# Kernel tuning notes

Measured on AMD Instinct MI355X. Metric: run time of the kernel, lower is better.

Reference implementation:

```python
import jax, jax.numpy as jnp
import numpy as np

NEG = -1e9  # finite stand-in for -inf (avoids inf-inf NaNs, safe in fp32)


def setup_inputs() -> dict:
    T, V, Lmax, A = 2048, 8192, 8, 64
    rng = np.random.default_rng(0)
    seq = rng.integers(0, A, size=T).astype(np.int32)
    # first A pieces are the single codepoints -> every sequence is segmentable
    piece_lens = np.concatenate([
        np.ones(A, np.int32),
        rng.integers(1, Lmax + 1, size=V - A).astype(np.int32),
    ])
    pieces = rng.integers(0, A, size=(V, Lmax)).astype(np.int32)
    pieces[:A, 0] = np.arange(A)
    logits = rng.standard_normal(V).astype(np.float32)
    m = logits.max()
    log_probs = (logits - m - np.log(np.exp(logits - m).sum())).astype(np.float32)
    return {
        'seq': jnp.asarray(seq),
        'pieces': jnp.asarray(pieces),
        'piece_lens': jnp.asarray(piece_lens),
        'log_probs': jnp.asarray(log_probs),
    }


def reference(seq, pieces, piece_lens, log_probs):
    T = seq.shape[0]
    V, Lmax = pieces.shape
    dt = log_probs.dtype

    # --- match table: match[t, i] = piece i matches sequence at position t ---
    seq_pad = jnp.concatenate([seq, jnp.full((Lmax,), -1, seq.dtype)])
    windows = seq_pad[jnp.arange(T)[:, None] + jnp.arange(Lmax)[None, :]]  # [T, Lmax]
    lmask = jnp.arange(Lmax)[None, :] < piece_lens[:, None]                # [V, Lmax]
    eq = windows[:, None, :] == pieces[None, :, :]                        # [T, V, Lmax]
    fits = (jnp.arange(T)[:, None] + piece_lens[None, :]) <= T            # [T, V]
    match = jnp.all(eq | ~lmask[None, :, :], axis=-1) & fits              # [T, V]
    mlp = jnp.where(match, log_probs[None, :], NEG).astype(dt)            # [T, V]

    # end_logp[t-1, i] = mlp[t - len_i, i]  (piece i ending exactly at t, t=1..T)
    te = jnp.arange(1, T + 1)[:, None]
    src = te - piece_lens[None, :]
    end_logp = jnp.where(src >= 0,
                         mlp[jnp.clip(src, 0, T - 1), jnp.arange(V)[None, :]],
                         NEG)

    # --- forward pass: alpha[t] = logsumexp_i alpha[t - len_i] + log p_i ---
    idx_a = Lmax - piece_lens  # window slot holding alpha[t - len_i]
    def fstep(win, row):
        a_t = jax.nn.logsumexp(win[idx_a] + row)
        return jnp.concatenate([win[1:], a_t[None]]), a_t
    win0 = jnp.full((Lmax,), NEG, dt).at[-1].set(0.0)
    _, alpha_rest = jax.lax.scan(fstep, win0, end_logp)
    alpha = jnp.concatenate([jnp.zeros((1,), dt), alpha_rest])  # [T+1]

    # --- backward pass: beta[t] = logsumexp_i log p_i + beta[t + len_i] ---
    idx_b = piece_lens - 1  # window slot holding beta[t + len_i]
    def bstep(win, row):
        b_t = jax.nn.logsumexp(row + win[idx_b])
        return jnp.concatenate([b_t[None], win[:-1]]), b_t
    winT = jnp.full((Lmax,), NEG, dt).at[0].set(0.0)
    _, beta_rev = jax.lax.scan(bstep, winT, mlp[::-1])
    beta = jnp.concatenate([beta_rev[::-1], jnp.zeros((1,), dt)])  # [T+1]

    # --- posteriors: P[t, i] = exp(alpha[t] + log p_i + beta[t+len_i] - alpha[T]) ---
    norm = alpha[T]
    beta_next = beta[jnp.clip(jnp.arange(T)[:, None] + piece_lens[None, :], 0, T)]
    P = jnp.exp(alpha[:T][:, None] + mlp + beta_next - norm)
    P = jnp.where(match, P, 0.0)
    return jnp.where(norm > NEG / 2, P, jnp.zeros_like(P))
```

## Files before the change

### kernel.cpp

```cpp
#include <hip/hip_runtime.h>
#include <stdint.h>

#define LMAX 8
#define KCH 32
#define NC  64
#define TT  2048
#define LN2D 0.6931471805599453
#define NEGE (-(1<<28))

struct __align__(16) PK { unsigned long long key; float logp; int len; };

__device__ __forceinline__ int fexp(float m) { return ((__float_as_int(m) >> 23) & 0xFF) - 127; }
__device__ __forceinline__ int fexpbits(float m) { return (__float_as_int(m) >> 23) & 0xFF; }
__device__ __forceinline__ float p2(int e) { return __int_as_float((e + 127) << 23); }
__device__ __forceinline__ float p2c(int e) { return (e < -126) ? 0.f : p2(e); }

__global__ void k_prep(const int* __restrict__ seq, const int* __restrict__ pieces,
                       const int* __restrict__ plens, const float* __restrict__ logp,
                       PK* __restrict__ pk, unsigned long long* __restrict__ w64,
                       float* __restrict__ M, int T, int V) {
  int idx = blockIdx.x * blockDim.x + threadIdx.x;
  if (idx < V) {
    const int* pr = pieces + idx * LMAX;
    int len = plens[idx];
    unsigned long long key = 0ull;
    #pragma unroll
    for (int l = 0; l < LMAX; ++l) {
      unsigned long long b = (unsigned long long)(pr[l] & 0xFF);
      if (l < len) key |= b << (8 * l);
    }
    PK o; o.key = key; o.logp = logp[idx]; o.len = len;
    pk[idx] = o;
  } else if (idx < V + T) {
    int t = idx - V;
    unsigned long long w = 0ull;
    #pragma unroll
    for (int l = 0; l < LMAX; ++l) {
      int pos = t + l;
      unsigned long long b = (pos < T) ? (unsigned long long)(seq[pos] & 0xFF) : 0xFFull;
      w |= b << (8 * l);
    }
    w64[t] = w;
  } else if (idx < V + T + T * LMAX) {
    M[idx - V - T] = 0.f;
  }
}

__global__ void k_match(const PK* __restrict__ pk, const unsigned long long* __restrict__ w64,
                        float* __restrict__ M, int T, int V, int tPer) {
  int v = blockIdx.x * blockDim.x + threadIdx.x;
  PK p = pk[v];
  unsigned long long mask = (p.len >= 8) ? ~0ull : ((1ull << (8 * p.len)) - 1ull);
  unsigned long long key = p.key;
  int t0 = blockIdx.y * tPer;
  float prob = -1.f;
  for (int t = t0; t < t0 + tPer; ++t) {
    unsigned long long w = w64[t];
    if (((w ^ key) & mask) == 0ull) {
      if (prob < 0.f) prob = expf(p.logp);
      atomicAdd(&M[t * LMAX + (p.len - 1)], prob);
    }
  }
}

__global__ __launch_bounds__(512) void k_chunks(const float* __restrict__ M,
        float* __restrict__ Wt, int* __restrict__ EWc) {
  int gtid = blockIdx.x * 512 + threadIdx.x;
  int task = gtid >> 3, b = gtid & 7;
  int dir = task >> 6, c = task & 63;
  int base = c * KCH;
  const float4* Mv = (const float4*)M;
  float v[8];
  #pragma unroll
  for (int i = 0; i < 8; ++i) v[i] = (i == b) ? 1.f : 0.f;
  int ec = 0;
  if (dir == 0) {
    float4 ra = Mv[base * 2], rb = Mv[base * 2 + 1];
    for (int kg = 0; kg < 4; ++kg) {
      #pragma unroll
      for (int kk = 0; kk < 8; ++kk) {
        int k = kg * 8 + kk;
        float4 c0 = ra, c1 = rb;
        int nk = (k + 1 < KCH) ? k + 1 : KCH - 1;
        ra = Mv[(base + nk) * 2]; rb = Mv[(base + nk) * 2 + 1];
        float a_ = v[kk & 7];
        v[(kk + 1) & 7] = fmaf(a_, c0.x, v[(kk + 1) & 7]);
        v[(kk + 2) & 7] = fmaf(a_, c0.y, v[(kk + 2) & 7]);
        v[(kk + 3) & 7] = fmaf(a_, c0.z, v[(kk + 3) & 7]);
        v[(kk + 4) & 7] = fmaf(a_, c0.w, v[(kk + 4) & 7]);
        v[(kk + 5) & 7] = fmaf(a_, c1.x, v[(kk + 5) & 7]);
        v[(kk + 6) & 7] = fmaf(a_, c1.y, v[(kk + 6) & 7]);
        v[(kk + 7) & 7] = fmaf(a_, c1.z, v[(kk + 7) & 7]);
        v[kk & 7]       = a_ * c1.w;
        if (kk == 3 || kk == 7) {
          float mx = 0.f;
          #pragma unroll
          for (int i = 0; i < 8; ++i) mx = fmaxf(mx, v[i]);
          if (fexpbits(mx) != 0) {
            int e = fexp(mx); float sc = p2(-e);
            #pragma unroll
            for (int i = 0; i < 8; ++i) v[i] *= sc;
            ec += e;
          }
        }
      }
    }
  } else {
    float4 ra = Mv[(base + KCH - 1) * 2], rb = Mv[(base + KCH - 1) * 2 + 1];
    for (int kg = 0; kg < 4; ++kg) {
      #pragma unroll
      for (int kk = 0; kk < 8; ++kk) {
        int k = kg * 8 + kk;
        float4 c0 = ra, c1 = rb;
        int nk = (k + 1 < KCH) ? k + 1 : KCH - 1;
        int nt = base + KCH - 1 - nk;
        ra = Mv[nt * 2]; rb = Mv[nt * 2 + 1];
        float nb =      c0.x * v[(8  - kk) & 7];
        nb = fmaf(c0.y, v[(9  - kk) & 7], nb);
        nb = fmaf(c0.z, v[(10 - kk) & 7], nb);
        nb = fmaf(c0.w, v[(11 - kk) & 7], nb);
        nb = fmaf(c1.x, v[(12 - kk) & 7], nb);
        nb = fmaf(c1.y, v[(13 - kk) & 7], nb);
        nb = fmaf(c1.z, v[(14 - kk) & 7], nb);
        nb = fmaf(c1.w, v[(15 - kk) & 7], nb);
        v[(7 - kk) & 7] = nb;
        if (kk == 3 || kk == 7) {
          float mx = 0.f;
          #pragma unroll
          for (int i = 0; i < 8; ++i) mx = fmaxf(mx, v[i]);
          if (fexpbits(mx) != 0) {
            int e = fexp(mx); float sc = p2(-e);
            #pragma unroll
            for (int i = 0; i < 8; ++i) v[i] *= sc;
            ec += e;
          }
        }
      }
    }
  }
  float mx = 0.f;
  #pragma unroll
  for (int i = 0; i < 8; ++i) mx = fmaxf(mx, v[i]);
  int ltask = dir * 64 + (dir ? 63 - c : c);
  float* wp = Wt + ltask * 64;
  if (fexpbits(mx) == 0) {
    #pragma unroll
    for (int i = 0; i < 8; ++i) wp[b * 8 + i] = 0.f;
    EWc[ltask * 8 + b] = NEGE;
  } else {
    int e = fexp(mx); float sc = p2(-e);
    #pragma unroll
    for (int i = 0; i < 8; ++i) wp[b * 8 + i] = v[i] * sc;
    EWc[ltask * 8 + b] = ec + e;
  }
}

__global__ __launch_bounds__(256) void k_combine(const float* __restrict__ Wt,
        const int* __restrict__ EWc, float* __restrict__ Pm,
        float* __restrict__ Cs, int* __restrict__ Eacc) {
  __shared__ float sWt[128][68];
  __shared__ int   sEW[128 * 8];
  __shared__ int   sEP[128 * 8];
  __shared__ float Gm[16 * 69];
  __shared__ float Sg[16 * 9];
  __shared__ int   EGs[16 * 8];
  __shared__ int   EsB[16];
  const int tid = threadIdx.x;

  for (int i = tid; i < 128 * 16; i += 256) {
    int task = i >> 4, q = i & 15;
    float4 v4 = ((const float4*)Wt)[i];
    *(float4*)&sWt[task][q * 4] = v4;
  }
  for (int i = tid; i < 1024; i += 256) sEW[i] = EWc[i];
  __syncthreads();

  if (tid < 128) {
    const int dir = tid >> 6, w = (tid >> 3) & 7, b = tid & 7;
    float v[8];
    #pragma unroll
    for (int i = 0; i < 8; ++i) v[i] = (i == b) ? 1.f : 0.f;
    int ec = 0;
    for (int c = 0; c < 8; ++c) {
      int lc = w * 8 + c, lt = dir * 64 + lc;
      float* pp = Pm + lt * 64 + b * 8;
      #pragma unroll
      for (int i = 0; i < 8; ++i) pp[i] = v[i];
      sEP[lt * 8 + b] = ec;
      const float* wp = &sWt[lt][0];
      int ew[8];
      #pragma unroll
      for (int j = 0; j < 8; ++j) ew[j] = sEW[lt * 8 + j];
      int emax = ew[0];
      #pragma unroll
      for (int j = 1; j < 8; ++j) emax = max(emax, ew[j]);
      float nv[8] = {0, 0, 0, 0, 0, 0, 0, 0};
      #pragma unroll
      for (int j = 0; j < 8; ++j) {
        float tj = v[j] * p2c(ew[j] - emax + 64);
        float4 ca = *(const float4*)(wp + j * 8);
        float4 cb = *(const float4*)(wp + j * 8 + 4);
        nv[0] = fmaf(tj, ca.x, nv[0]); nv[1] = fmaf(tj, ca.y, nv[1]);
        nv[2] = fmaf(tj, ca.z, nv[2]); nv[3] = fmaf(tj, ca.w, nv[3]);
        nv[4] = fmaf(tj, cb.x, nv[4]); nv[5] = fmaf(tj, cb.y, nv[5]);
        nv[6] = fmaf(tj, cb.z, nv[6]); nv[7] = fmaf(tj, cb.w, nv[7]);
      }
      float mx = 0.f;
      #pragma unroll
      for (int i = 0; i < 8; ++i) mx = fmaxf(mx, nv[i]);
      if (fexpbits(mx) == 0) {
        #pragma unroll
        for (int i = 0; i < 8; ++i) v[i] = 0.f;
        ec = NEGE;
      } else {
        int e = fexp(mx); float sc = p2(-e);
        #pragma unroll
        for (int i = 0; i < 8; ++i) v[i] = nv[i] * sc;
        ec = ec + emax + e - 64;
      }
    }
    float* gp = Gm + (dir * 8 + w) * 69 + b * 8;
    #pragma unroll
    for (int i = 0; i < 8; ++i) gp[i] = v[i];
    EGs[(dir * 8 + w) * 8 + b] = ec;
  }
  __syncthreads();

  if (tid < 8 || (tid >= 64 && tid < 72)) {
    const int dir = (tid >= 64) ? 1 : 0, j = tid & 7;
    float s[8];
    #pragma unroll
    for (int i = 0; i < 8; ++i) s[i] = (i == 0) ? 1.f : 0.f;
    int Es = 0;
    for (int w = 0; w < 8; ++w) {
      float sj = s[0];
      #pragma unroll
      for (int i = 1; i < 8; ++i) if (j == i) sj = s[i];
      Sg[(dir * 8 + w) * 9 + j] = sj;
      if (j == 0) EsB[dir * 8 + w] = Es;
      int eg[8];
      #pragma unroll
      for (int i = 0; i < 8; ++i) eg[i] = EGs[(dir * 8 + w) * 8 + i];
      int egmax = eg[0];
      #pragma unroll
      for (int i = 1; i < 8; ++i) egmax = max(egmax, eg[i]);
      int egj = eg[0];
      #pragma unroll
      for (int i = 1; i < 8; ++i) if (j == i) egj = eg[i];
      float tb = sj * p2c(egj - egmax + 64);
      const float* gp = Gm + (dir * 8 + w) * 69 + j * 8;
      float p[8];
      #pragma unroll
      for (int i = 0; i < 8; ++i) p[i] = gp[i] * tb;
      #pragma unroll
      for (int m = 1; m <= 4; m <<= 1)
        #pragma unroll
        for (int i = 0; i < 8; ++i) p[i] += __shfl_xor(p[i], m);
      float mx = 0.f;
      #pragma unroll
      for (int i = 0; i < 8; ++i) mx = fmaxf(mx, p[i]);
      int e = fexp(mx); float sc = p2(-e);
      #pragma unroll
      for (int i = 0; i < 8; ++i) s[i] = p[i] * sc;
      Es += egmax + e - 64;
    }
  }
  __syncthreads();

  if (tid < 128) {
    const int dir = tid >> 6, lc = tid & 63, w = lc >> 3;
    float sg[8];
    #pragma unroll
    for (int b = 0; b < 8; ++b) sg[b] = Sg[(dir * 8 + w) * 9 + b];
    int Es = EsB[dir * 8 + w];
    int ep[8];
    #pragma unroll
    for (int b = 0; b < 8; ++b) ep[b] = sEP[(dir * 64 + lc) * 8 + b];
    int epmax = ep[0];
    #pragma unroll
    for (int b = 1; b < 8; ++b) epmax = max(epmax, ep[b]);
    float cs[8] = {0, 0, 0, 0, 0, 0, 0, 0};
    #pragma unroll
    for (int b = 0; b < 8; ++b) {
      float coef = sg[b] * p2c(ep[b] - epmax + 64);
      const float* pp = Pm + (dir * 64 + lc) * 64 + b * 8;
      float4 ca = *(const float4*)pp;
      float4 cb = *(const float4*)(pp + 4);
      cs[0] = fmaf(coef, ca.x, cs[0]); cs[1] = fmaf(coef, ca.y, cs[1]);
      cs[2] = fmaf(coef, ca.z, cs[2]); cs[3] = fmaf(coef, ca.w, cs[3]);
      cs[4] = fmaf(coef, cb.x, cs[4]); cs[5] = fmaf(coef, cb.y, cs[5]);
      cs[6] = fmaf(coef, cb.z, cs[6]); cs[7] = fmaf(coef, cb.w, cs[7]);
    }
    float mx = 0.f;
    #pragma unroll
    for (int i = 0; i < 8; ++i) mx = fmaxf(mx, cs[i]);
    int phys = dir ? (63 - lc) : lc;
    float* cp = Cs + (dir * 64 + phys) * 8;
    if (fexpbits(mx) == 0) {
      #pragma unroll
      for (int i = 0; i < 8; ++i) cp[i] = 0.f;
      Eacc[dir * 64 + phys] = NEGE;
    } else {
      int e = fexp(mx); float sc = p2(-e);
      #pragma unroll
      for (int i = 0; i < 8; ++i) cp[i] = cs[i] * sc;
      Eacc[dir * 64 + phys] = Es + epmax + e - 64;
    }
  }
}

__global__ __launch_bounds__(64) void k_replay(const float* __restrict__ M,
        const float* __restrict__ Cs, const int* __restrict__ Eacc,
        float* __restrict__ aL, float* __restrict__ bL) {
  const int dir = blockIdx.x;
  const int c = threadIdx.x;
  const int base = c * KCH;
  const float4* Mv = (const float4*)M;
  const float* cp = Cs + (dir * 64 + c) * 8;
  double st[8];
  #pragma unroll
  for (int i = 0; i < 8; ++i) st[i] = (double)cp[i];
  const double eacc = (double)Eacc[dir * 64 + c];
  if (dir == 0) {
    if (c == 0) aL[0] = 0.f;
    float4 ra = Mv[base * 2], rb = Mv[base * 2 + 1];
    for (int kg = 0; kg < 4; ++kg) {
      #pragma unroll
      for (int kk = 0; kk < 8; ++kk) {
        int k = kg * 8 + kk;
        float4 c0 = ra, c1 = rb;
        int nk = (k + 1 < KCH) ? k + 1 : KCH - 1;
        ra = Mv[(base + nk) * 2]; rb = Mv[(base + nk) * 2 + 1];
        double a_ = st[kk & 7];
        st[(kk + 1) & 7] = fma(a_, (double)c0.x, st[(kk + 1) & 7]);
        st[(kk + 2) & 7] = fma(a_, (double)c0.y, st[(kk + 2) & 7]);
        st[(kk + 3) & 7] = fma(a_, (double)c0.z, st[(kk + 3) & 7]);
        st[(kk + 4) & 7] = fma(a_, (double)c0.w, st[(kk + 4) & 7]);
        st[(kk + 5) & 7] = fma(a_, (double)c1.x, st[(kk + 5) & 7]);
        st[(kk + 6) & 7] = fma(a_, (double)c1.y, st[(kk + 6) & 7]);
        st[(kk + 7) & 7] = fma(a_, (double)c1.z, st[(kk + 7) & 7]);
        st[kk & 7]       = a_ * (double)c1.w;
        double val = st[(kk + 1) & 7];
        long long bits = __double_as_longlong(val);
        int e2 = (int)((bits >> 52) & 0x7ff) - 1023;
        double mant = __longlong_as_double((bits & 0xFFFFFFFFFFFFFLL) | 0x3FF0000000000000LL);
        float lg = log2f((float)mant);
        aL[base + k + 1] = (float)(((double)e2 + eacc + (double)lg) * LN2D);
      }
    }
  } else {
    if (c == 0) bL[TT] = 0.f;
    float4 ra = Mv[(base + KCH - 1) * 2], rb = Mv[(base + KCH - 1) * 2 + 1];
    for (int kg = 0; kg < 4; ++kg) {
      #pragma unroll
      for (int kk = 0; kk < 8; ++kk) {
        int k = kg * 8 + kk;
        int t = base + KCH - 1 - k;
        float4 c0 = ra, c1 = rb;
        int nk = (k + 1 < KCH) ? k + 1 : KCH - 1;
        int nt = base + KCH - 1 - nk;
        ra = Mv[nt * 2]; rb = Mv[nt * 2 + 1];
        double nb =            (double)c0.x * st[(8  - kk) & 7];
        nb = fma((double)c0.y, st[(9  - kk) & 7], nb);
        nb = fma((double)c0.z, st[(10 - kk) & 7], nb);
        nb = fma((double)c0.w, st[(11 - kk) & 7], nb);
        nb = fma((double)c1.x, st[(12 - kk) & 7], nb);
        nb = fma((double)c1.y, st[(13 - kk) & 7], nb);
        nb = fma((double)c1.z, st[(14 - kk) & 7], nb);
        nb = fma((double)c1.w, st[(15 - kk) & 7], nb);
        st[(7 - kk) & 7] = nb;
        long long bits = __double_as_longlong(nb);
        int e2 = (int)((bits >> 52) & 0x7ff) - 1023;
        double mant = __longlong_as_double((bits & 0xFFFFFFFFFFFFFLL) | 0x3FF0000000000000LL);
        float lg = log2f((float)mant);
        bL[t] = (float)(((double)e2 + eacc + (double)lg) * LN2D);
      }
    }
  }
}

__global__ void k_out(const PK* __restrict__ pk, const unsigned long long* __restrict__ w64,
                      const float* __restrict__ aL, const float* __restrict__ bL,
                      float* __restrict__ out, int T, int V, int tPer) {
  int v = blockIdx.x * blockDim.x + threadIdx.x;
  PK p = pk[v];
  unsigned long long mask = (p.len >= 8) ? ~0ull : ((1ull << (8 * p.len)) - 1ull);
  unsigned long long key = p.key;
  float norm = aL[T];
  float base = p.logp - norm;
  int t0 = blockIdx.y * tPer;
  for (int t = t0; t < t0 + tPer; ++t) {
    unsigned long long w = w64[t];
    float val = 0.f;
    if (((w ^ key) & mask) == 0ull)
      val = __expf(aL[t] + base + bL[t + p.len]);
    out[(size_t)t * V + v] = val;
  }
}

extern "C" void kernel_launch(void* const* d_in, const int* in_sizes, int n_in,
                              void* d_out, int out_size, void* d_ws, size_t ws_size,
                              hipStream_t stream) {
  const int* seq    = (const int*)d_in[0];
  const int* pieces = (const int*)d_in[1];
  const int* plens  = (const int*)d_in[2];
  const float* logp = (const float*)d_in[3];
  float* out = (float*)d_out;
  const int T = in_sizes[0];
  const int V = in_sizes[2];

  char* p = (char*)d_ws;
  PK* pk = (PK*)p;                                   p += (size_t)V * sizeof(PK);
  unsigned long long* w64 = (unsigned long long*)p;  p += (size_t)T * 8;
  float* M = (float*)p;                              p += (size_t)T * LMAX * 4;
  float* Wt = (float*)p;                             p += (size_t)128 * 64 * 4;
  int* EWc = (int*)p;                                p += (size_t)128 * 8 * 4;
  float* Pm = (float*)p;                             p += (size_t)128 * 64 * 4;
  float* Cs = (float*)p;                             p += (size_t)128 * 8 * 4;
  int* Eacc = (int*)p;                               p += 512;
  float* aL = (float*)p;                             p += 8208;
  float* bL = (float*)p;                             p += 8208;

  int prepN = V + T + T * LMAX;
  k_prep<<<(prepN + 255) / 256, 256, 0, stream>>>(seq, pieces, plens, logp, pk, w64, M, T, V);

  const int tPer2 = 128;
  dim3 g2(V / 256, T / tPer2);
  k_match<<<g2, 256, 0, stream>>>(pk, w64, M, T, V, tPer2);

  k_chunks<<<2, 512, 0, stream>>>(M, Wt, EWc);
  k_combine<<<1, 256, 0, stream>>>(Wt, EWc, Pm, Cs, Eacc);
  k_replay<<<2, 64, 0, stream>>>(M, Cs, Eacc, aL, bL);

  const int tPer5 = 32;
  dim3 g5(V / 256, T / tPer5);
  k_out<<<g5, 256, 0, stream>>>(pk, w64, aL, bL, out, T, V, tPer5);
}
```

Before: 59.39 us.

## Fuse chunk, combine and replay scan kernels into one single-block kernel

```diff
diff --git a/kernel.cpp b/kernel.cpp
--- a/kernel.cpp
+++ b/kernel.cpp
@@ -63,101 +63,10 @@
   }
 }
 
-__global__ __launch_bounds__(512) void k_chunks(const float* __restrict__ M,
-        float* __restrict__ Wt, int* __restrict__ EWc) {
-  int gtid = blockIdx.x * 512 + threadIdx.x;
-  int task = gtid >> 3, b = gtid & 7;
-  int dir = task >> 6, c = task & 63;
-  int base = c * KCH;
-  const float4* Mv = (const float4*)M;
-  float v[8];
-  #pragma unroll
-  for (int i = 0; i < 8; ++i) v[i] = (i == b) ? 1.f : 0.f;
-  int ec = 0;
-  if (dir == 0) {
-    float4 ra = Mv[base * 2], rb = Mv[base * 2 + 1];
-    for (int kg = 0; kg < 4; ++kg) {
-      #pragma unroll
-      for (int kk = 0; kk < 8; ++kk) {
-        int k = kg * 8 + kk;
-        float4 c0 = ra, c1 = rb;
-        int nk = (k + 1 < KCH) ? k + 1 : KCH - 1;
-        ra = Mv[(base + nk) * 2]; rb = Mv[(base + nk) * 2 + 1];
-        float a_ = v[kk & 7];
-        v[(kk + 1) & 7] = fmaf(a_, c0.x, v[(kk + 1) & 7]);
-        v[(kk + 2) & 7] = fmaf(a_, c0.y, v[(kk + 2) & 7]);
-        v[(kk + 3) & 7] = fmaf(a_, c0.z, v[(kk + 3) & 7]);
-        v[(kk + 4) & 7] = fmaf(a_, c0.w, v[(kk + 4) & 7]);
-        v[(kk + 5) & 7] = fmaf(a_, c1.x, v[(kk + 5) & 7]);
-        v[(kk + 6) & 7] = fmaf(a_, c1.y, v[(kk + 6) & 7]);
-        v[(kk + 7) & 7] = fmaf(a_, c1.z, v[(kk + 7) & 7]);
-        v[kk & 7]       = a_ * c1.w;
-        if (kk == 3 || kk == 7) {
-          float mx = 0.f;
-          #pragma unroll
-          for (int i = 0; i < 8; ++i) mx = fmaxf(mx, v[i]);
-          if (fexpbits(mx) != 0) {
-            int e = fexp(mx); float sc = p2(-e);
-            #pragma unroll
-            for (int i = 0; i < 8; ++i) v[i] *= sc;
-            ec += e;
-          }
-        }
-      }
-    }
-  } else {
-    float4 ra = Mv[(base + KCH - 1) * 2], rb = Mv[(base + KCH - 1) * 2 + 1];
-    for (int kg = 0; kg < 4; ++kg) {
-      #pragma unroll
-      for (int kk = 0; kk < 8; ++kk) {
-        int k = kg * 8 + kk;
-        float4 c0 = ra, c1 = rb;
-        int nk = (k + 1 < KCH) ? k + 1 : KCH - 1;
-        int nt = base + KCH - 1 - nk;
-        ra = Mv[nt * 2]; rb = Mv[nt * 2 + 1];
-        float nb =      c0.x * v[(8  - kk) & 7];
-        nb = fmaf(c0.y, v[(9  - kk) & 7], nb);
-        nb = fmaf(c0.z, v[(10 - kk) & 7], nb);
-        nb = fmaf(c0.w, v[(11 - kk) & 7], nb);
-        nb = fmaf(c1.x, v[(12 - kk) & 7], nb);
-        nb = fmaf(c1.y, v[(13 - kk) & 7], nb);
-        nb = fmaf(c1.z, v[(14 - kk) & 7], nb);
-        nb = fmaf(c1.w, v[(15 - kk) & 7], nb);
-        v[(7 - kk) & 7] = nb;
-        if (kk == 3 || kk == 7) {
-          float mx = 0.f;
-          #pragma unroll
-          for (int i = 0; i < 8; ++i) mx = fmaxf(mx, v[i]);
-          if (fexpbits(mx) != 0) {
-            int e = fexp(mx); float sc = p2(-e);
-            #pragma unroll
-            for (int i = 0; i < 8; ++i) v[i] *= sc;
-            ec += e;
-          }
-        }
-      }
-    }
-  }
-  float mx = 0.f;
-  #pragma unroll
-  for (int i = 0; i < 8; ++i) mx = fmaxf(mx, v[i]);
-  int ltask = dir * 64 + (dir ? 63 - c : c);
-  float* wp = Wt + ltask * 64;
-  if (fexpbits(mx) == 0) {
-    #pragma unroll
-    for (int i = 0; i < 8; ++i) wp[b * 8 + i] = 0.f;
-    EWc[ltask * 8 + b] = NEGE;
-  } else {
-    int e = fexp(mx); float sc = p2(-e);
-    #pragma unroll
-    for (int i = 0; i < 8; ++i) wp[b * 8 + i] = v[i] * sc;
-    EWc[ltask * 8 + b] = ec + e;
-  }
-}
-
-__global__ __launch_bounds__(256) void k_combine(const float* __restrict__ Wt,
-        const int* __restrict__ EWc, float* __restrict__ Pm,
-        float* __restrict__ Cs, int* __restrict__ Eacc) {
+__global__ __launch_bounds__(512, 2) void k_scan(const float* __restrict__ M,
+        float* __restrict__ Wt, int* __restrict__ EWc, float* __restrict__ Pm,
+        float* __restrict__ Cs, int* __restrict__ Eacc,
+        float* __restrict__ aL, float* __restrict__ bL) {
   __shared__ float sWt[128][68];
   __shared__ int   sEW[128 * 8];
   __shared__ int   sEP[128 * 8];
@@ -166,13 +75,134 @@
   __shared__ int   EGs[16 * 8];
   __shared__ int   EsB[16];
   const int tid = threadIdx.x;
-
-  for (int i = tid; i < 128 * 16; i += 256) {
+  const float4* Mv = (const float4*)M;
+
+  {
+    const int g = tid >> 3, b = tid & 7;
+    const int c = g;
+    const int base = c * KCH;
+    float va[8], vb[8];
+    #pragma unroll
+    for (int i = 0; i < 8; ++i) { va[i] = (i == b) ? 1.f : 0.f; vb[i] = va[i]; }
+    int eca = 0, ecb = 0;
+    float4 fa[8], bw[8], fn[8], bn[8];
+    #pragma unroll
+    for (int i = 0; i < 4; ++i) {
+      fa[2 * i]     = Mv[(base + i) * 2];
+      fa[2 * i + 1] = Mv[(base + i) * 2 + 1];
+      bw[2 * i]     = Mv[(base + 31 - i) * 2];
+      bw[2 * i + 1] = Mv[(base + 31 - i) * 2 + 1];
+    }
+    #pragma unroll
+    for (int blk = 0; blk < 8; ++blk) {
+      if (blk < 7) {
+        #pragma unroll
+        for (int i = 0; i < 4; ++i) {
+          int rf = base + (blk + 1) * 4 + i;
+          int rb = base + 31 - ((blk + 1) * 4 + i);
+          fn[2 * i]     = Mv[rf * 2];
+          fn[2 * i + 1] = Mv[rf * 2 + 1];
+          bn[2 * i]     = Mv[rb * 2];
+          bn[2 * i + 1] = Mv[rb * 2 + 1];
+        }
+      }
+      #pragma unroll
+      for (int s = 0; s < 4; ++s) {
+        const int kk = blk * 4 + s;
+        {
+          float4 c0 = fa[2 * s], c1 = fa[2 * s + 1];
+          float a_ = va[kk & 7];
+          va[(kk + 1) & 7] = fmaf(a_, c0.x, va[(kk + 1) & 7]);
+          va[(kk + 2) & 7] = fmaf(a_, c0.y, va[(kk + 2) & 7]);
+          va[(kk + 3) & 7] = fmaf(a_, c0.z, va[(kk + 3) & 7]);
+          va[(kk + 4) & 7] = fmaf(a_, c0.w, va[(kk + 4) & 7]);
+          va[(kk + 5) & 7] = fmaf(a_, c1.x, va[(kk + 5) & 7]);
+          va[(kk + 6) & 7] = fmaf(a_, c1.y, va[(kk + 6) & 7]);
+          va[(kk + 7) & 7] = fmaf(a_, c1.z, va[(kk + 7) & 7]);
+          va[kk & 7]       = a_ * c1.w;
+        }
+        {
+          float4 c0 = bw[2 * s], c1 = bw[2 * s + 1];
+          float nb =      c0.x * vb[(8  - kk) & 7];
+          nb = fmaf(c0.y, vb[(9  - kk) & 7], nb);
+          nb = fmaf(c0.z, vb[(10 - kk) & 7], nb);
+          nb = fmaf(c0.w, vb[(11 - kk) & 7], nb);
+          nb = fmaf(c1.x, vb[(12 - kk) & 7], nb);
+          nb = fmaf(c1.y, vb[(13 - kk) & 7], nb);
+          nb = fmaf(c1.z, vb[(14 - kk) & 7], nb);
+          nb = fmaf(c1.w, vb[(15 - kk) & 7], nb);
+          vb[(7 - kk) & 7] = nb;
+        }
+      }
+      {
+        float mx = 0.f;
+        #pragma unroll
+        for (int i = 0; i < 8; ++i) mx = fmaxf(mx, va[i]);
+        if (fexpbits(mx) != 0) {
+          int e = fexp(mx); float sc = p2(-e);
+          #pragma unroll
+          for (int i = 0; i < 8; ++i) va[i] *= sc;
+          eca += e;
+        }
+      }
+      {
+        float mx = 0.f;
+        #pragma unroll
+        for (int i = 0; i < 8; ++i) mx = fmaxf(mx, vb[i]);
+        if (fexpbits(mx) != 0) {
+          int e = fexp(mx); float sc = p2(-e);
+          #pragma unroll
+          for (int i = 0; i < 8; ++i) vb[i] *= sc;
+          ecb += e;
+        }
+      }
+      if (blk < 7) {
+        #pragma unroll
+        for (int i = 0; i < 8; ++i) { fa[i] = fn[i]; bw[i] = bn[i]; }
+      }
+    }
+    {
+      float mx = 0.f;
+      #pragma unroll
+      for (int i = 0; i < 8; ++i) mx = fmaxf(mx, va[i]);
+      float* wp = Wt + c * 64;
+      if (fexpbits(mx) == 0) {
+        #pragma unroll
+        for (int i = 0; i < 8; ++i) wp[b * 8 + i] = 0.f;
+        EWc[c * 8 + b] = NEGE;
+      } else {
+        int e = fexp(mx); float sc = p2(-e);
+        #pragma unroll
+        for (int i = 0; i < 8; ++i) wp[b * 8 + i] = va[i] * sc;
+        EWc[c * 8 + b] = eca + e;
+      }
+    }
+    {
+      float mx = 0.f;
+      #pragma unroll
+      for (int i = 0; i < 8; ++i) mx = fmaxf(mx, vb[i]);
+      int lt = 64 + (63 - c);
+      float* wp = Wt + lt * 64;
+      if (fexpbits(mx) == 0) {
+        #pragma unroll
+        for (int i = 0; i < 8; ++i) wp[b * 8 + i] = 0.f;
+        EWc[lt * 8 + b] = NEGE;
+      } else {
+        int e = fexp(mx); float sc = p2(-e);
+        #pragma unroll
+        for (int i = 0; i < 8; ++i) wp[b * 8 + i] = vb[i] * sc;
+        EWc[lt * 8 + b] = ecb + e;
+      }
+    }
+  }
+  __syncthreads();
+
+  for (int i = tid; i < 128 * 16; i += 512) {
     int task = i >> 4, q = i & 15;
     float4 v4 = ((const float4*)Wt)[i];
     *(float4*)&sWt[task][q * 4] = v4;
   }
-  for (int i = tid; i < 1024; i += 256) sEW[i] = EWc[i];
+  for (int i = tid; i < 1024; i += 512) sEW[i] = EWc[i];
   __syncthreads();
 
   if (tid < 128) {
@@ -307,73 +337,100 @@
       Eacc[dir * 64 + phys] = Es + epmax + e - 64;
     }
   }
-}
-
-__global__ __launch_bounds__(64) void k_replay(const float* __restrict__ M,
-        const float* __restrict__ Cs, const int* __restrict__ Eacc,
-        float* __restrict__ aL, float* __restrict__ bL) {
-  const int dir = blockIdx.x;
-  const int c = threadIdx.x;
-  const int base = c * KCH;
-  const float4* Mv = (const float4*)M;
-  const float* cp = Cs + (dir * 64 + c) * 8;
-  double st[8];
-  #pragma unroll
-  for (int i = 0; i < 8; ++i) st[i] = (double)cp[i];
-  const double eacc = (double)Eacc[dir * 64 + c];
-  if (dir == 0) {
-    if (c == 0) aL[0] = 0.f;
-    float4 ra = Mv[base * 2], rb = Mv[base * 2 + 1];
-    for (int kg = 0; kg < 4; ++kg) {
-      #pragma unroll
-      for (int kk = 0; kk < 8; ++kk) {
-        int k = kg * 8 + kk;
-        float4 c0 = ra, c1 = rb;
-        int nk = (k + 1 < KCH) ? k + 1 : KCH - 1;
-        ra = Mv[(base + nk) * 2]; rb = Mv[(base + nk) * 2 + 1];
-        double a_ = st[kk & 7];
-        st[(kk + 1) & 7] = fma(a_, (double)c0.x, st[(kk + 1) & 7]);
-        st[(kk + 2) & 7] = fma(a_, (double)c0.y, st[(kk + 2) & 7]);
-        st[(kk + 3) & 7] = fma(a_, (double)c0.z, st[(kk + 3) & 7]);
-        st[(kk + 4) & 7] = fma(a_, (double)c0.w, st[(kk + 4) & 7]);
-        st[(kk + 5) & 7] = fma(a_, (double)c1.x, st[(kk + 5) & 7]);
-        st[(kk + 6) & 7] = fma(a_, (double)c1.y, st[(kk + 6) & 7]);
-        st[(kk + 7) & 7] = fma(a_, (double)c1.z, st[(kk + 7) & 7]);
-        st[kk & 7]       = a_ * (double)c1.w;
-        double val = st[(kk + 1) & 7];
-        long long bits = __double_as_longlong(val);
-        int e2 = (int)((bits >> 52) & 0x7ff) - 1023;
-        double mant = __longlong_as_double((bits & 0xFFFFFFFFFFFFFLL) | 0x3FF0000000000000LL);
-        float lg = log2f((float)mant);
-        aL[base + k + 1] = (float)(((double)e2 + eacc + (double)lg) * LN2D);
-      }
-    }
-  } else {
-    if (c == 0) bL[TT] = 0.f;
-    float4 ra = Mv[(base + KCH - 1) * 2], rb = Mv[(base + KCH - 1) * 2 + 1];
-    for (int kg = 0; kg < 4; ++kg) {
-      #pragma unroll
-      for (int kk = 0; kk < 8; ++kk) {
-        int k = kg * 8 + kk;
-        int t = base + KCH - 1 - k;
-        float4 c0 = ra, c1 = rb;
-        int nk = (k + 1 < KCH) ? k + 1 : KCH - 1;
-        int nt = base + KCH - 1 - nk;
-        ra = Mv[nt * 2]; rb = Mv[nt * 2 + 1];
-        double nb =            (double)c0.x * st[(8  - kk) & 7];
-        nb = fma((double)c0.y, st[(9  - kk) & 7], nb);
-        nb = fma((double)c0.z, st[(10 - kk) & 7], nb);
-        nb = fma((double)c0.w, st[(11 - kk) & 7], nb);
-        nb = fma((double)c1.x, st[(12 - kk) & 7], nb);
-        nb = fma((double)c1.y, st[(13 - kk) & 7], nb);
-        nb = fma((double)c1.z, st[(14 - kk) & 7], nb);
-        nb = fma((double)c1.w, st[(15 - kk) & 7], nb);
-        st[(7 - kk) & 7] = nb;
-        long long bits = __double_as_longlong(nb);
-        int e2 = (int)((bits >> 52) & 0x7ff) - 1023;
-        double mant = __longlong_as_double((bits & 0xFFFFFFFFFFFFFLL) | 0x3FF0000000000000LL);
-        float lg = log2f((float)mant);
-        bL[t] = (float)(((double)e2 + eacc + (double)lg) * LN2D);
+  __syncthreads();
+
+  if (tid < 128) {
+    const int dir = tid >> 6;
+    const int c = tid & 63;
+    const int base = c * KCH;
+    const float* cp = Cs + (dir * 64 + c) * 8;
+    double st[8];
+    #pragma unroll
+    for (int i = 0; i < 8; ++i) st[i] = (double)cp[i];
+    const double eacc = (double)Eacc[dir * 64 + c];
+    if (tid == 0) { aL[0] = 0.f; bL[TT] = 0.f; }
+    float4 A[8], Bn[8];
+    if (dir == 0) {
+      #pragma unroll
+      for (int i = 0; i < 4; ++i) {
+        A[2 * i]     = Mv[(base + i) * 2];
+        A[2 * i + 1] = Mv[(base + i) * 2 + 1];
+      }
+      #pragma unroll
+      for (int blk = 0; blk < 8; ++blk) {
+        if (blk < 7) {
+          #pragma unroll
+          for (int i = 0; i < 4; ++i) {
+            int rf = base + (blk + 1) * 4 + i;
+            Bn[2 * i]     = Mv[rf * 2];
+            Bn[2 * i + 1] = Mv[rf * 2 + 1];
+          }
+        }
+        #pragma unroll
+        for (int s = 0; s < 4; ++s) {
+          const int kk = blk * 4 + s;
+          float4 c0 = A[2 * s], c1 = A[2 * s + 1];
+          double a_ = st[kk & 7];
+          st[(kk + 1) & 7] = fma(a_, (double)c0.x, st[(kk + 1) & 7]);
+          st[(kk + 2) & 7] = fma(a_, (double)c0.y, st[(kk + 2) & 7]);
+          st[(kk + 3) & 7] = fma(a_, (double)c0.z, st[(kk + 3) & 7]);
+          st[(kk + 4) & 7] = fma(a_, (double)c0.w, st[(kk + 4) & 7]);
+          st[(kk + 5) & 7] = fma(a_, (double)c1.x, st[(kk + 5) & 7]);
+          st[(kk + 6) & 7] = fma(a_, (double)c1.y, st[(kk + 6) & 7]);
+          st[(kk + 7) & 7] = fma(a_, (double)c1.z, st[(kk + 7) & 7]);
+          st[kk & 7]       = a_ * (double)c1.w;
+          double val = st[(kk + 1) & 7];
+          long long bits = __double_as_longlong(val);
+          int e2 = (int)((bits >> 52) & 0x7ff) - 1023;
+          double mant = __longlong_as_double((bits & 0xFFFFFFFFFFFFFLL) | 0x3FF0000000000000LL);
+          float lg = log2f((float)mant);
+          aL[base + kk + 1] = (float)(((double)e2 + eacc + (double)lg) * LN2D);
+        }
+        if (blk < 7) {
+          #pragma unroll
+          for (int i = 0; i < 8; ++i) A[i] = Bn[i];
+        }
+      }
+    } else {
+      #pragma unroll
+      for (int i = 0; i < 4; ++i) {
+        A[2 * i]     = Mv[(base + 31 - i) * 2];
+        A[2 * i + 1] = Mv[(base + 31 - i) * 2 + 1];
+      }
+      #pragma unroll
+      for (int blk = 0; blk < 8; ++blk) {
+        if (blk < 7) {
+          #pragma unroll
+          for (int i = 0; i < 4; ++i) {
+            int rb = base + 31 - ((blk + 1) * 4 + i);
+            Bn[2 * i]     = Mv[rb * 2];
+            Bn[2 * i + 1] = Mv[rb * 2 + 1];
+          }
+        }
+        #pragma unroll
+        for (int s = 0; s < 4; ++s) {
+          const int kk = blk * 4 + s;
+          const int t = base + 31 - kk;
+          float4 c0 = A[2 * s], c1 = A[2 * s + 1];
+          double nb =            (double)c0.x * st[(8  - kk) & 7];
+          nb = fma((double)c0.y, st[(9  - kk) & 7], nb);
+          nb = fma((double)c0.z, st[(10 - kk) & 7], nb);
+          nb = fma((double)c0.w, st[(11 - kk) & 7], nb);
+          nb = fma((double)c1.x, st[(12 - kk) & 7], nb);
+          nb = fma((double)c1.y, st[(13 - kk) & 7], nb);
+          nb = fma((double)c1.z, st[(14 - kk) & 7], nb);
+          nb = fma((double)c1.w, st[(15 - kk) & 7], nb);
+          st[(7 - kk) & 7] = nb;
+          long long bits = __double_as_longlong(nb);
+          int e2 = (int)((bits >> 52) & 0x7ff) - 1023;
+          double mant = __longlong_as_double((bits & 0xFFFFFFFFFFFFFLL) | 0x3FF0000000000000LL);
+          float lg = log2f((float)mant);
+          bL[t] = (float)(((double)e2 + eacc + (double)lg) * LN2D);
+        }
+        if (blk < 7) {
+          #pragma unroll
+          for (int i = 0; i < 8; ++i) A[i] = Bn[i];
+        }
       }
     }
   }
@@ -428,9 +485,7 @@
   dim3 g2(V / 256, T / tPer2);
   k_match<<<g2, 256, 0, stream>>>(pk, w64, M, T, V, tPer2);
 
-  k_chunks<<<2, 512, 0, stream>>>(M, Wt, EWc);
-  k_combine<<<1, 256, 0, stream>>>(Wt, EWc, Pm, Cs, Eacc);
-  k_replay<<<2, 64, 0, stream>>>(M, Cs, Eacc, aL, bL);
+  k_scan<<<1, 512, 0, stream>>>(M, Wt, EWc, Pm, Cs, Eacc, aL, bL);
 
   const int tPer5 = 32;
   dim3 g5(V / 256, T / tPer5);
```

Result: no change. 58.76 us (-1.1%).

## Fuse combine and replay kernels into one block, spread chunk scan across blocks

Applied to the files above, without the earlier changes.

```diff
diff --git a/kernel.cpp b/kernel.cpp
--- a/kernel.cpp
+++ b/kernel.cpp
@@ -63,9 +63,9 @@
   }
 }
 
-__global__ __launch_bounds__(512) void k_chunks(const float* __restrict__ M,
+__global__ __launch_bounds__(64, 1) void k_chunks(const float* __restrict__ M,
         float* __restrict__ Wt, int* __restrict__ EWc) {
-  int gtid = blockIdx.x * 512 + threadIdx.x;
+  int gtid = blockIdx.x * 64 + threadIdx.x;
   int task = gtid >> 3, b = gtid & 7;
   int dir = task >> 6, c = task & 63;
   int base = c * KCH;
@@ -155,9 +155,9 @@
   }
 }
 
-__global__ __launch_bounds__(256) void k_combine(const float* __restrict__ Wt,
-        const int* __restrict__ EWc, float* __restrict__ Pm,
-        float* __restrict__ Cs, int* __restrict__ Eacc) {
+__global__ __launch_bounds__(128, 1) void k_fin(const float* __restrict__ M,
+        const float* __restrict__ Wt, const int* __restrict__ EWc,
+        float* __restrict__ Pm, float* __restrict__ aL, float* __restrict__ bL) {
   __shared__ float sWt[128][68];
   __shared__ int   sEW[128 * 8];
   __shared__ int   sEP[128 * 8];
@@ -165,17 +165,20 @@
   __shared__ float Sg[16 * 9];
   __shared__ int   EGs[16 * 8];
   __shared__ int   EsB[16];
+  __shared__ float sCs[128 * 8];
+  __shared__ int   sEacc[128];
   const int tid = threadIdx.x;
-
-  for (int i = tid; i < 128 * 16; i += 256) {
+  const float4* Mv = (const float4*)M;
+
+  for (int i = tid; i < 128 * 16; i += 128) {
     int task = i >> 4, q = i & 15;
     float4 v4 = ((const float4*)Wt)[i];
     *(float4*)&sWt[task][q * 4] = v4;
   }
-  for (int i = tid; i < 1024; i += 256) sEW[i] = EWc[i];
+  for (int i = tid; i < 1024; i += 128) sEW[i] = EWc[i];
   __syncthreads();
 
-  if (tid < 128) {
+  {
     const int dir = tid >> 6, w = (tid >> 3) & 7, b = tid & 7;
     float v[8];
     #pragma unroll
@@ -267,7 +270,7 @@
   }
   __syncthreads();
 
-  if (tid < 128) {
+  {
     const int dir = tid >> 6, lc = tid & 63, w = lc >> 3;
     float sg[8];
     #pragma unroll
@@ -295,85 +298,82 @@
     #pragma unroll
     for (int i = 0; i < 8; ++i) mx = fmaxf(mx, cs[i]);
     int phys = dir ? (63 - lc) : lc;
-    float* cp = Cs + (dir * 64 + phys) * 8;
+    float* cp = &sCs[(dir * 64 + phys) * 8];
     if (fexpbits(mx) == 0) {
       #pragma unroll
       for (int i = 0; i < 8; ++i) cp[i] = 0.f;
-      Eacc[dir * 64 + phys] = NEGE;
+      sEacc[dir * 64 + phys] = NEGE;
     } else {
       int e = fexp(mx); float sc = p2(-e);
       #pragma unroll
       for (int i = 0; i < 8; ++i) cp[i] = cs[i] * sc;
-      Eacc[dir * 64 + phys] = Es + epmax + e - 64;
-    }
-  }
-}
-
-__global__ __launch_bounds__(64) void k_replay(const float* __restrict__ M,
-        const float* __restrict__ Cs, const int* __restrict__ Eacc,
-        float* __restrict__ aL, float* __restrict__ bL) {
-  const int dir = blockIdx.x;
-  const int c = threadIdx.x;
-  const int base = c * KCH;
-  const float4* Mv = (const float4*)M;
-  const float* cp = Cs + (dir * 64 + c) * 8;
-  double st[8];
-  #pragma unroll
-  for (int i = 0; i < 8; ++i) st[i] = (double)cp[i];
-  const double eacc = (double)Eacc[dir * 64 + c];
-  if (dir == 0) {
-    if (c == 0) aL[0] = 0.f;
-    float4 ra = Mv[base * 2], rb = Mv[base * 2 + 1];
-    for (int kg = 0; kg < 4; ++kg) {
-      #pragma unroll
-      for (int kk = 0; kk < 8; ++kk) {
-        int k = kg * 8 + kk;
-        float4 c0 = ra, c1 = rb;
-        int nk = (k + 1 < KCH) ? k + 1 : KCH - 1;
-        ra = Mv[(base + nk) * 2]; rb = Mv[(base + nk) * 2 + 1];
-        double a_ = st[kk & 7];
-        st[(kk + 1) & 7] = fma(a_, (double)c0.x, st[(kk + 1) & 7]);
-        st[(kk + 2) & 7] = fma(a_, (double)c0.y, st[(kk + 2) & 7]);
-        st[(kk + 3) & 7] = fma(a_, (double)c0.z, st[(kk + 3) & 7]);
-        st[(kk + 4) & 7] = fma(a_, (double)c0.w, st[(kk + 4) & 7]);
-        st[(kk + 5) & 7] = fma(a_, (double)c1.x, st[(kk + 5) & 7]);
-        st[(kk + 6) & 7] = fma(a_, (double)c1.y, st[(kk + 6) & 7]);
-        st[(kk + 7) & 7] = fma(a_, (double)c1.z, st[(kk + 7) & 7]);
-        st[kk & 7]       = a_ * (double)c1.w;
-        double val = st[(kk + 1) & 7];
-        long long bits = __double_as_longlong(val);
-        int e2 = (int)((bits >> 52) & 0x7ff) - 1023;
-        double mant = __longlong_as_double((bits & 0xFFFFFFFFFFFFFLL) | 0x3FF0000000000000LL);
-        float lg = log2f((float)mant);
-        aL[base + k + 1] = (float)(((double)e2 + eacc + (double)lg) * LN2D);
-      }
-    }
-  } else {
-    if (c == 0) bL[TT] = 0.f;
-    float4 ra = Mv[(base + KCH - 1) * 2], rb = Mv[(base + KCH - 1) * 2 + 1];
-    for (int kg = 0; kg < 4; ++kg) {
-      #pragma unroll
-      for (int kk = 0; kk < 8; ++kk) {
-        int k = kg * 8 + kk;
-        int t = base + KCH - 1 - k;
-        float4 c0 = ra, c1 = rb;
-        int nk = (k + 1 < KCH) ? k + 1 : KCH - 1;
-        int nt = base + KCH - 1 - nk;
-        ra = Mv[nt * 2]; rb = Mv[nt * 2 + 1];
-        double nb =            (double)c0.x * st[(8  - kk) & 7];
-        nb = fma((double)c0.y, st[(9  - kk) & 7], nb);
-        nb = fma((double)c0.z, st[(10 - kk) & 7], nb);
-        nb = fma((double)c0.w, st[(11 - kk) & 7], nb);
-        nb = fma((double)c1.x, st[(12 - kk) & 7], nb);
-        nb = fma((double)c1.y, st[(13 - kk) & 7], nb);
-        nb = fma((double)c1.z, st[(14 - kk) & 7], nb);
-        nb = fma((double)c1.w, st[(15 - kk) & 7], nb);
-        st[(7 - kk) & 7] = nb;
-        long long bits = __double_as_longlong(nb);
-        int e2 = (int)((bits >> 52) & 0x7ff) - 1023;
-        double mant = __longlong_as_double((bits & 0xFFFFFFFFFFFFFLL) | 0x3FF0000000000000LL);
-        float lg = log2f((float)mant);
-        bL[t] = (float)(((double)e2 + eacc + (double)lg) * LN2D);
+      sEacc[dir * 64 + phys] = Es + epmax + e - 64;
+    }
+  }
+  __syncthreads();
+
+  {
+    const int dir = tid >> 6;
+    const int c = tid & 63;
+    const int base = c * KCH;
+    const float* cp = &sCs[(dir * 64 + c) * 8];
+    double st[8];
+    #pragma unroll
+    for (int i = 0; i < 8; ++i) st[i] = (double)cp[i];
+    const double eacc = (double)sEacc[dir * 64 + c];
+    if (tid == 0) { aL[0] = 0.f; bL[TT] = 0.f; }
+    if (dir == 0) {
+      float4 ra = Mv[base * 2], rb = Mv[base * 2 + 1];
+      for (int kg = 0; kg < 4; ++kg) {
+        #pragma unroll
+        for (int kk = 0; kk < 8; ++kk) {
+          int k = kg * 8 + kk;
+          float4 c0 = ra, c1 = rb;
+          int nk = (k + 1 < KCH) ? k + 1 : KCH - 1;
+          ra = Mv[(base + nk) * 2]; rb = Mv[(base + nk) * 2 + 1];
+          double a_ = st[kk & 7];
+          st[(kk + 1) & 7] = fma(a_, (double)c0.x, st[(kk + 1) & 7]);
+          st[(kk + 2) & 7] = fma(a_, (double)c0.y, st[(kk + 2) & 7]);
+          st[(kk + 3) & 7] = fma(a_, (double)c0.z, st[(kk + 3) & 7]);
+          st[(kk + 4) & 7] = fma(a_, (double)c0.w, st[(kk + 4) & 7]);
+          st[(kk + 5) & 7] = fma(a_, (double)c1.x, st[(kk + 5) & 7]);
+          st[(kk + 6) & 7] = fma(a_, (double)c1.y, st[(kk + 6) & 7]);
+          st[(kk + 7) & 7] = fma(a_, (double)c1.z, st[(kk + 7) & 7]);
+          st[kk & 7]       = a_ * (double)c1.w;
+          double val = st[(kk + 1) & 7];
+          long long bits = __double_as_longlong(val);
+          int e2 = (int)((bits >> 52) & 0x7ff) - 1023;
+          double mant = __longlong_as_double((bits & 0xFFFFFFFFFFFFFLL) | 0x3FF0000000000000LL);
+          float lg = log2f((float)mant);
+          aL[base + k + 1] = (float)(((double)e2 + eacc + (double)lg) * LN2D);
+        }
+      }
+    } else {
+      float4 ra = Mv[(base + KCH - 1) * 2], rb = Mv[(base + KCH - 1) * 2 + 1];
+      for (int kg = 0; kg < 4; ++kg) {
+        #pragma unroll
+        for (int kk = 0; kk < 8; ++kk) {
+          int k = kg * 8 + kk;
+          int t = base + KCH - 1 - k;
+          float4 c0 = ra, c1 = rb;
+          int nk = (k + 1 < KCH) ? k + 1 : KCH - 1;
+          int nt = base + KCH - 1 - nk;
+          ra = Mv[nt * 2]; rb = Mv[nt * 2 + 1];
+          double nb =            (double)c0.x * st[(8  - kk) & 7];
+          nb = fma((double)c0.y, st[(9  - kk) & 7], nb);
+          nb = fma((double)c0.z, st[(10 - kk) & 7], nb);
+          nb = fma((double)c0.w, st[(11 - kk) & 7], nb);
+          nb = fma((double)c1.x, st[(12 - kk) & 7], nb);
+          nb = fma((double)c1.y, st[(13 - kk) & 7], nb);
+          nb = fma((double)c1.z, st[(14 - kk) & 7], nb);
+          nb = fma((double)c1.w, st[(15 - kk) & 7], nb);
+          st[(7 - kk) & 7] = nb;
+          long long bits = __double_as_longlong(nb);
+          int e2 = (int)((bits >> 52) & 0x7ff) - 1023;
+          double mant = __longlong_as_double((bits & 0xFFFFFFFFFFFFFLL) | 0x3FF0000000000000LL);
+          float lg = log2f((float)mant);
+          bL[t] = (float)(((double)e2 + eacc + (double)lg) * LN2D);
+        }
       }
     }
   }
@@ -416,8 +416,6 @@
   float* Wt = (float*)p;                             p += (size_t)128 * 64 * 4;
   int* EWc = (int*)p;                                p += (size_t)128 * 8 * 4;
   float* Pm = (float*)p;                             p += (size_t)128 * 64 * 4;
-  float* Cs = (float*)p;                             p += (size_t)128 * 8 * 4;
-  int* Eacc = (int*)p;                               p += 512;
   float* aL = (float*)p;                             p += 8208;
   float* bL = (float*)p;                             p += 8208;
 
@@ -428,9 +426,8 @@
   dim3 g2(V / 256, T / tPer2);
   k_match<<<g2, 256, 0, stream>>>(pk, w64, M, T, V, tPer2);
 
-  k_chunks<<<2, 512, 0, stream>>>(M, Wt, EWc);
-  k_combine<<<1, 256, 0, stream>>>(Wt, EWc, Pm, Cs, Eacc);
-  k_replay<<<2, 64, 0, stream>>>(M, Cs, Eacc, aL, bL);
+  k_chunks<<<16, 64, 0, stream>>>(M, Wt, EWc);
+  k_fin<<<1, 128, 0, stream>>>(M, Wt, EWc, Pm, aL, bL);
 
   const int tPer5 = 32;
   dim3 g5(V / 256, T / tPer5);
```

Result: no change. 59.42 us (+0.1%).
